# Kernel optimization log

Hardware: AMD Instinct MI355X
Metric: run time of the kernel (lower is better)

## Reference

```python
import jax, jax.numpy as jnp
import numpy as np

EPS = 1e-12

def l2norm(x, axis):
    # torch.nn.functional.normalize: x / max(||x||_2, eps)
    n = jnp.sqrt(jnp.sum(x * x, axis=axis, keepdims=True))
    return x / jnp.maximum(n, EPS)

def setup_inputs() -> dict:
    key = jax.random.key(0)
    k1, k2, k3, k4 = jax.random.split(key, 4)
    B, Cf, H, W = 128, 1024, 16, 16
    n_att, dv = 312, 300
    img = jax.random.normal(k1, (B, Cf, H, W), dtype=jnp.float32)
    # V is initialized from row-normalized w2v embeddings in the module
    V = l2norm(jax.random.normal(k2, (n_att, dv), dtype=jnp.float32), axis=1)
    W1 = jax.random.normal(k3, (dv, Cf), dtype=jnp.float32)
    W2 = jax.random.normal(k4, (dv, Cf), dtype=jnp.float32)
    return {"img": img, "V": V, "W1": W1, "W2": W2}

def reference(img, V, W1, W2):
    vv = l2norm(V, axis=1)                               # [i, v]
    B, Cf, H, Wd = img.shape
    av = l2norm(img.reshape(B, Cf, H * Wd), axis=1)      # [b, f, r]
    Q = vv @ W1                                          # [i, f]
    A = jnp.einsum('if,bfr->bir', Q, av)                 # attention logits
    A = jax.nn.softmax(A, axis=-1)
    F_p = jnp.einsum('bir,bfr->bif', A, av)              # attended features
    Pred_att = jnp.einsum('if,bif->bi', vv @ W2, F_p)
    return Pred_att
```

## Files before the change

### kernel.cpp

```cpp
#include <hip/hip_runtime.h>
#include <math.h>

#define NB   128
#define CF   1024
#define RR   256
#define NA   312
#define DV   300
#define MT   640
#define NKC  32
#define NQ   160

typedef _Float16 half8  __attribute__((ext_vector_type(8)));
typedef _Float16 half4  __attribute__((ext_vector_type(4)));
typedef float float16v  __attribute__((ext_vector_type(16)));
typedef float float4v   __attribute__((ext_vector_type(4)));

__device__ __forceinline__ void gll16(const void* g, void* l) {
    __builtin_amdgcn_global_load_lds(
        (const __attribute__((address_space(1))) void*)g,
        (__attribute__((address_space(3))) void*)l, 16, 0, 0);
}

__launch_bounds__(256, 4)
__global__ void k_prep(const float* __restrict__ img, float* __restrict__ ssq32,
                       _Float16* __restrict__ avT) {
    int m  = blockIdx.x;
    int kc = m & 31;
    int b  = m >> 5;
    int t  = threadIdx.x;
    __shared__ __align__(16) float tile[32][256];

    const char* src = (const char*)(img + ((size_t)b * CF + kc * 32) * RR);
    #pragma unroll
    for (int i = 0; i < 8; ++i)
        gll16(src + (size_t)i * 4096 + (size_t)t * 16,
              (char*)tile + i * 4096 + t * 16);
    asm volatile("s_waitcnt vmcnt(0)" ::: "memory");
    __syncthreads();

    float v[32];
    #pragma unroll
    for (int f = 0; f < 32; ++f) v[f] = tile[f][t];
    float ss = 0.f;
    #pragma unroll
    for (int f = 0; f < 32; ++f) ss += v[f] * v[f];

    _Float16* dst = avT + ((size_t)(b * NKC + kc) * RR + t) * 32;
    #pragma unroll
    for (int s = 0; s < 4; ++s) {
        half8 o;
        #pragma unroll
        for (int j = 0; j < 8; ++j) o[j] = (_Float16)v[s * 8 + j];
        *(half8*)(dst + s * 8) = o;
    }
    ssq32[(size_t)(b * NKC + kc) * RR + t] = ss;
}

__launch_bounds__(256, 4)
__global__ void k_q(const float* __restrict__ V, const float* __restrict__ W1,
                    const float* __restrict__ W2, _Float16* __restrict__ Qb) {
    int ib = blockIdx.x;
    int t  = threadIdx.x;
    bool isQ2 = ib >= 80;
    int i0l = (ib - (isQ2 ? 80 : 0)) * 4;
    __shared__ float inv4[4];
    float acc[4][4];
    #pragma unroll
    for (int ii = 0; ii < 4; ++ii)
        #pragma unroll
        for (int j = 0; j < 4; ++j) acc[ii][j] = 0.f;
    if (i0l < NA) {
        int row = t >> 6, l64 = t & 63;
        float s = 0.f;
        for (int v = l64; v < DV; v += 64) { float x = V[(i0l + row) * DV + v]; s += x * x; }
        #pragma unroll
        for (int o = 32; o; o >>= 1) s += __shfl_xor(s, o, 64);
        if (l64 == 0) inv4[row] = 1.f / fmaxf(sqrtf(s), 1e-12f);
        __syncthreads();
        const float* W  = isQ2 ? W2 : W1;
        const float* Vb = V + (size_t)i0l * DV;
        for (int v = 0; v < DV; v += 2) {
            float4v w0 = *(const float4v*)(W + (size_t)v * CF + t * 4);
            float4v w1 = *(const float4v*)(W + (size_t)(v + 1) * CF + t * 4);
            #pragma unroll
            for (int ii = 0; ii < 4; ++ii) {
                float a0 = Vb[(size_t)ii * DV + v];
                float a1 = Vb[(size_t)ii * DV + v + 1];
                #pragma unroll
                for (int j = 0; j < 4; ++j) acc[ii][j] += a0 * w0[j] + a1 * w1[j];
            }
        }
        #pragma unroll
        for (int ii = 0; ii < 4; ++ii)
            #pragma unroll
            for (int j = 0; j < 4; ++j) acc[ii][j] *= inv4[ii];
    }
    int fg = t >> 3;
    int fo = (t & 7) * 4;
    int q12 = isQ2 ? 1 : 0;
    #pragma unroll
    for (int ii = 0; ii < 4; ++ii) {
        half4 h;
        #pragma unroll
        for (int j = 0; j < 4; ++j) h[j] = (_Float16)acc[ii][j];
        *(half4*)&Qb[((size_t)fg * MT + (2 * (i0l + ii) + q12)) * 32 + fo] = h;
    }
}

extern __shared__ char smem[];
__launch_bounds__(512, 2)
__global__ void k_gemm(const _Float16* __restrict__ Qb, const _Float16* __restrict__ avT,
                       const float* __restrict__ ssq32, float* __restrict__ out) {
    int lin = blockIdx.x;
    int xcd = lin & 7;
    int u   = lin >> 3;
    int b   = xcd + 8 * (u & 15);
    int t2h = u >> 4;

    int tid  = threadIdx.x;
    int lane = tid & 63;
    int w    = tid >> 6;
    int wm   = w >> 2;
    int wn   = w & 3;
    int nl   = lane & 31;
    int kh   = lane >> 5;

    int c1 = 512 + tid;
    int a_s0 = (tid % 320) * 64 + (tid / 320) * 16;
    int a_s1 = (c1 % 320) * 64 + (c1 / 320) * 16;
    int a_s2 = ((tid & 255) + 64) * 64 + 3 * 16;
    int a_d0 = tid * 16;
    int a_d1 = a_d0 + 8192;
    int a_d2 = 16384 + (tid & 255) * 16;
    int b_s0 = (tid & 255) * 64 + (tid >> 8) * 16;

    const char* Abase_g = (const char*)Qb;
    const char* Bbase_g = (const char*)avT + ((size_t)b * NKC) * RR * 64;

    float16v acc[5][2];
    #pragma unroll
    for (int i = 0; i < 5; ++i)
        #pragma unroll
        for (int j = 0; j < 2; ++j)
            #pragma unroll
            for (int gi = 0; gi < 16; ++gi) acc[i][j][gi] = 0.f;

    char* p0 = smem;
    char* p1 = smem + 36864;
    char* p2 = smem + 73728;

    #define STAGE(kc_, buf) do {                                                   \
        int kcl = (kc_) < NKC ? (kc_) : (NKC - 1);                                 \
        const char* aS = Abase_g + ((size_t)kcl * MT + (size_t)t2h * 320) * 64;    \
        const char* bS = Bbase_g + (size_t)kcl * RR * 64;                          \
        char* ab = (buf); char* bb = (buf) + 20480;                                \
        gll16(aS + a_s0, ab + a_d0);                                               \
        gll16(aS + a_s1, ab + a_d1);                                               \
        gll16(aS + a_s2, ab + a_d2);                                               \
        gll16(bS + b_s0,      bb + tid * 16);                                      \
        gll16(bS + b_s0 + 32, bb + tid * 16 + 8192);                               \
    } while (0)

    #define COMPUTE(buf) do {                                                      \
        const char* Al = (buf); const char* Bl = (buf) + 20480;                    \
        _Pragma("unroll")                                                          \
        for (int ks = 0; ks < 2; ++ks) {                                           \
            int kb = ks * 2 + kh;                                                  \
            half8 bf0 = *(const half8*)(Bl + ((size_t)kb * 256 + wn * 64 + nl) * 16);      \
            half8 bf1 = *(const half8*)(Bl + ((size_t)kb * 256 + wn * 64 + 32 + nl) * 16); \
            _Pragma("unroll")                                                      \
            for (int mt = 0; mt < 5; ++mt) {                                       \
                half8 af = *(const half8*)(Al + ((size_t)kb * 320 + wm * 160 + mt * 32 + nl) * 16); \
                acc[mt][0] = __builtin_amdgcn_mfma_f32_32x32x16_f16(af, bf0, acc[mt][0], 0, 0, 0);  \
                acc[mt][1] = __builtin_amdgcn_mfma_f32_32x32x16_f16(af, bf1, acc[mt][1], 0, 0, 0);  \
            }                                                                      \
        }                                                                          \
    } while (0)

    STAGE(0, p0);
    __builtin_amdgcn_sched_barrier(0);
    STAGE(1, p1);
    asm volatile("s_waitcnt vmcnt(5)" ::: "memory");
    __builtin_amdgcn_s_barrier();
    __builtin_amdgcn_sched_barrier(0);

    #pragma unroll 1
    for (int kc = 0; kc < NKC; ++kc) {
        STAGE(kc + 2, p2);
        asm volatile("s_waitcnt vmcnt(5)" ::: "memory");
        __builtin_amdgcn_sched_barrier(0);
        COMPUTE(p0);
        __builtin_amdgcn_sched_barrier(0);
        __builtin_amdgcn_s_barrier();
        char* tmp = p0; p0 = p1; p1 = p2; p2 = tmp;
    }
    asm volatile("s_waitcnt vmcnt(0)" ::: "memory");
    __builtin_amdgcn_s_barrier();
    __builtin_amdgcn_sched_barrier(0);
    #undef STAGE
    #undef COMPUTE

    float* mred = (float*)smem;
    float* mg   = (float*)(smem + 2560);
    float* sred = (float*)(smem + 3200);
    float* dred = (float*)(smem + 5760);

    const float* sq = ssq32 + (size_t)b * NKC * RR;
    int c0 = wn * 64 + nl;
    float q0 = 0.f, q1 = 0.f;
    #pragma unroll
    for (int kc = 0; kc < NKC; ++kc) {
        q0 += sq[(size_t)kc * RR + c0];
        q1 += sq[(size_t)kc * RR + 32 + c0];
    }
    float iv0 = 1.f / fmaxf(sqrtf(q0), 1e-12f);
    float iv1 = 1.f / fmaxf(sqrtf(q1), 1e-12f);
    #pragma unroll
    for (int mt = 0; mt < 5; ++mt)
        #pragma unroll
        for (int gi = 0; gi < 16; ++gi) {
            acc[mt][0][gi] *= iv0;
            acc[mt][1][gi] *= iv1;
        }

    #pragma unroll
    for (int mt = 0; mt < 5; ++mt) {
        #pragma unroll
        for (int e = 0; e < 8; ++e) {
            int g = 2 * e;
            float mx = fmaxf(acc[mt][0][g], acc[mt][1][g]);
            #pragma unroll
            for (int off = 1; off <= 16; off <<= 1)
                mx = fmaxf(mx, __shfl_xor(mx, off, 64));
            if (nl == 0) {
                int row = (g & 3) + 8 * (g >> 2) + 4 * kh;
                mred[wn * 160 + wm * 80 + mt * 16 + (row >> 1)] = mx;
            }
        }
    }
    __syncthreads();
    if (tid < 160)
        mg[tid] = fmaxf(fmaxf(mred[tid], mred[160 + tid]),
                        fmaxf(mred[320 + tid], mred[480 + tid]));
    __syncthreads();

    #pragma unroll
    for (int mt = 0; mt < 5; ++mt) {
        #pragma unroll
        for (int e = 0; e < 8; ++e) {
            int g = 2 * e;
            int row = (g & 3) + 8 * (g >> 2) + 4 * kh;
            int Pl = wm * 80 + mt * 16 + (row >> 1);
            float m = mg[Pl];
            float e0 = __expf(acc[mt][0][g] - m);
            float e1 = __expf(acc[mt][1][g] - m);
            float s = e0 + e1;
            float d = e0 * acc[mt][0][g + 1] + e1 * acc[mt][1][g + 1];
            #pragma unroll
            for (int off = 1; off <= 16; off <<= 1) {
                s += __shfl_xor(s, off, 64);
                d += __shfl_xor(d, off, 64);
            }
            if (nl == 0) {
                sred[wn * 160 + Pl] = s;
                dred[wn * 160 + Pl] = d;
            }
        }
    }
    __syncthreads();
    if (tid < 160) {
        float s = sred[tid] + sred[160 + tid] + sred[320 + tid] + sred[480 + tid];
        float d = dred[tid] + dred[160 + tid] + dred[320 + tid] + dred[480 + tid];
        int ig = t2h * 160 + tid;
        if (ig < NA) out[b * NA + ig] = d / s;
    }
}

extern "C" void kernel_launch(void* const* d_in, const int* in_sizes, int n_in,
                              void* d_out, int out_size, void* d_ws, size_t ws_size,
                              hipStream_t stream) {
    const float* img = (const float*)d_in[0];
    const float* V   = (const float*)d_in[1];
    const float* W1  = (const float*)d_in[2];
    const float* W2  = (const float*)d_in[3];
    float* out = (float*)d_out;

    char* ws = (char*)d_ws;
    size_t off = 0;
    float*    ssq32 = (float*)(ws + off);    off += (size_t)NB * NKC * RR * 4;
    _Float16* avT   = (_Float16*)(ws + off); off += (size_t)NB * CF * RR * 2;
    _Float16* Qb    = (_Float16*)(ws + off); off += (size_t)NKC * MT * 32 * 2;

    static bool attr_done = false;
    if (!attr_done) {
        hipFuncSetAttribute((const void*)k_gemm,
                            hipFuncAttributeMaxDynamicSharedMemorySize, 110592);
        attr_done = true;
    }

    k_prep<<<dim3(NB * NKC), 256, 0, stream>>>(img, ssq32, avT);
    k_q<<<dim3(NQ), 256, 0, stream>>>(V, W1, W2, Qb);
    k_gemm<<<dim3(256), 512, 110592, stream>>>(Qb, avT, ssq32, out);
}
```

Before: 298.5 us.

## Fuse img fp16 conversion and norm into GEMM with split-R softmax combine

Removes the prep kernel that wrote an fp16 transposed copy of img plus per-chunk sums of squares. The GEMM kernel now streams fp32 img directly into LDS, converts it to fp16 in registers, and accumulates the column sums of squares itself. Each block now covers all 640 Q rows but only half of the 256 spatial positions. A small combine kernel merges the two halves' partial softmax max, sum and dot values. This saves a full write and re-read of the fp16 intermediate but doubles LDS traffic for B, adds scalar LDS reads and conversions to the inner loop, and drops from triple to double buffering.

```diff
diff --git a/kernel.cpp b/kernel.cpp
--- a/kernel.cpp
+++ b/kernel.cpp
@@ -9,6 +9,10 @@
 #define MT   640
 #define NKC  32
 #define NQ   160
+#define NPI  320
+#define ABYTES 40960
+#define BBYTES 16384
+#define BUFSZ  57344
 
 typedef _Float16 half8  __attribute__((ext_vector_type(8)));
 typedef _Float16 half4  __attribute__((ext_vector_type(4)));
@@ -19,41 +23,6 @@
     __builtin_amdgcn_global_load_lds(
         (const __attribute__((address_space(1))) void*)g,
         (__attribute__((address_space(3))) void*)l, 16, 0, 0);
-}
-
-__launch_bounds__(256, 4)
-__global__ void k_prep(const float* __restrict__ img, float* __restrict__ ssq32,
-                       _Float16* __restrict__ avT) {
-    int m  = blockIdx.x;
-    int kc = m & 31;
-    int b  = m >> 5;
-    int t  = threadIdx.x;
-    __shared__ __align__(16) float tile[32][256];
-
-    const char* src = (const char*)(img + ((size_t)b * CF + kc * 32) * RR);
-    #pragma unroll
-    for (int i = 0; i < 8; ++i)
-        gll16(src + (size_t)i * 4096 + (size_t)t * 16,
-              (char*)tile + i * 4096 + t * 16);
-    asm volatile("s_waitcnt vmcnt(0)" ::: "memory");
-    __syncthreads();
-
-    float v[32];
-    #pragma unroll
-    for (int f = 0; f < 32; ++f) v[f] = tile[f][t];
-    float ss = 0.f;
-    #pragma unroll
-    for (int f = 0; f < 32; ++f) ss += v[f] * v[f];
-
-    _Float16* dst = avT + ((size_t)(b * NKC + kc) * RR + t) * 32;
-    #pragma unroll
-    for (int s = 0; s < 4; ++s) {
-        half8 o;
-        #pragma unroll
-        for (int j = 0; j < 8; ++j) o[j] = (_Float16)v[s * 8 + j];
-        *(half8*)(dst + s * 8) = o;
-    }
-    ssq32[(size_t)(b * NKC + kc) * RR + t] = ss;
 }
 
 __launch_bounds__(256, 4)
@@ -109,33 +78,35 @@
 
 extern __shared__ char smem[];
 __launch_bounds__(512, 2)
-__global__ void k_gemm(const _Float16* __restrict__ Qb, const _Float16* __restrict__ avT,
-                       const float* __restrict__ ssq32, float* __restrict__ out) {
+__global__ void k_fused(const float* __restrict__ img, const _Float16* __restrict__ Qb,
+                        float* __restrict__ pm, float* __restrict__ ps,
+                        float* __restrict__ pd) {
     int lin = blockIdx.x;
-    int xcd = lin & 7;
-    int u   = lin >> 3;
-    int b   = xcd + 8 * (u & 15);
-    int t2h = u >> 4;
+    int b   = lin >> 1;
+    int rh  = lin & 1;
 
     int tid  = threadIdx.x;
     int lane = tid & 63;
     int w    = tid >> 6;
-    int wm   = w >> 2;
-    int wn   = w & 3;
+    int wm   = w >> 1;
+    int wn   = w & 1;
     int nl   = lane & 31;
     int kh   = lane >> 5;
 
-    int c1 = 512 + tid;
-    int a_s0 = (tid % 320) * 64 + (tid / 320) * 16;
-    int a_s1 = (c1 % 320) * 64 + (c1 / 320) * 16;
-    int a_s2 = ((tid & 255) + 64) * 64 + 3 * 16;
-    int a_d0 = tid * 16;
-    int a_d1 = a_d0 + 8192;
-    int a_d2 = 16384 + (tid & 255) * 16;
-    int b_s0 = (tid & 255) * 64 + (tid >> 8) * 16;
-
-    const char* Abase_g = (const char*)Qb;
-    const char* Bbase_g = (const char*)avT + ((size_t)b * NKC) * RR * 64;
+    int aG[5];
+    #pragma unroll
+    for (int j = 0; j < 5; ++j) {
+        int s = tid + j * 512;
+        aG[j] = ((s % 640) * 4 + (s / 640)) * 16;
+    }
+    int bG[2];
+    #pragma unroll
+    for (int j = 0; j < 2; ++j) {
+        int s = tid + j * 512;
+        bG[j] = (s >> 5) * (RR * 4) + (s & 31) * 16;
+    }
+    const char* gA = (const char*)Qb;
+    const char* gB = (const char*)img + ((size_t)b * CF * RR + (size_t)rh * 128) * 4;
 
     float16v acc[5][2];
     #pragma unroll
@@ -144,55 +115,67 @@
         for (int j = 0; j < 2; ++j)
             #pragma unroll
             for (int gi = 0; gi < 16; ++gi) acc[i][j][gi] = 0.f;
-
-    char* p0 = smem;
-    char* p1 = smem + 36864;
-    char* p2 = smem + 73728;
-
-    #define STAGE(kc_, buf) do {                                                   \
+    float ssq = 0.f;
+
+    #define STAGE(kc_) do {                                                        \
         int kcl = (kc_) < NKC ? (kc_) : (NKC - 1);                                 \
-        const char* aS = Abase_g + ((size_t)kcl * MT + (size_t)t2h * 320) * 64;    \
-        const char* bS = Bbase_g + (size_t)kcl * RR * 64;                          \
-        char* ab = (buf); char* bb = (buf) + 20480;                                \
-        gll16(aS + a_s0, ab + a_d0);                                               \
-        gll16(aS + a_s1, ab + a_d1);                                               \
-        gll16(aS + a_s2, ab + a_d2);                                               \
-        gll16(bS + b_s0,      bb + tid * 16);                                      \
-        gll16(bS + b_s0 + 32, bb + tid * 16 + 8192);                               \
+        char* buf = smem + (((kc_) & 1) ? BUFSZ : 0);                              \
+        const char* aS = gA + (size_t)kcl * ABYTES;                                \
+        const char* bS = gB + (size_t)kcl * 32768;                                 \
+        _Pragma("unroll")                                                          \
+        for (int j = 0; j < 5; ++j) gll16(aS + aG[j], buf + (tid + j * 512) * 16); \
+        _Pragma("unroll")                                                          \
+        for (int j = 0; j < 2; ++j)                                                \
+            gll16(bS + bG[j], buf + ABYTES + (tid + j * 512) * 16);                \
     } while (0)
 
-    #define COMPUTE(buf) do {                                                      \
-        const char* Al = (buf); const char* Bl = (buf) + 20480;                    \
+    #define COMPUTE(kc_) do {                                                      \
+        char* buf = smem + (((kc_) & 1) ? BUFSZ : 0);                              \
+        const char* Al = buf; const char* Bl = buf + ABYTES;                       \
+        int c0 = wn * 64 + nl;                                                     \
         _Pragma("unroll")                                                          \
         for (int ks = 0; ks < 2; ++ks) {                                           \
             int kb = ks * 2 + kh;                                                  \
-            half8 bf0 = *(const half8*)(Bl + ((size_t)kb * 256 + wn * 64 + nl) * 16);      \
-            half8 bf1 = *(const half8*)(Bl + ((size_t)kb * 256 + wn * 64 + 32 + nl) * 16); \
+            float bv0[8], bv1[8];                                                  \
+            _Pragma("unroll")                                                      \
+            for (int j = 0; j < 8; ++j) {                                          \
+                bv0[j] = *(const float*)(Bl + (((kb * 8 + j) * 128) + c0) * 4);    \
+                bv1[j] = *(const float*)(Bl + (((kb * 8 + j) * 128) + c0 + 32) * 4); \
+            }                                                                      \
+            half8 bf0, bf1;                                                        \
+            _Pragma("unroll")                                                      \
+            for (int j = 0; j < 8; ++j) {                                          \
+                bf0[j] = (_Float16)bv0[j]; bf1[j] = (_Float16)bv1[j];              \
+            }                                                                      \
             _Pragma("unroll")                                                      \
             for (int mt = 0; mt < 5; ++mt) {                                       \
-                half8 af = *(const half8*)(Al + ((size_t)kb * 320 + wm * 160 + mt * 32 + nl) * 16); \
+                half8 af = *(const half8*)(Al + ((size_t)kb * 640 + wm * 160 + mt * 32 + nl) * 16); \
                 acc[mt][0] = __builtin_amdgcn_mfma_f32_32x32x16_f16(af, bf0, acc[mt][0], 0, 0, 0);  \
                 acc[mt][1] = __builtin_amdgcn_mfma_f32_32x32x16_f16(af, bf1, acc[mt][1], 0, 0, 0);  \
             }                                                                      \
         }                                                                          \
     } while (0)
 
-    STAGE(0, p0);
-    __builtin_amdgcn_sched_barrier(0);
-    STAGE(1, p1);
-    asm volatile("s_waitcnt vmcnt(5)" ::: "memory");
-    __builtin_amdgcn_s_barrier();
-    __builtin_amdgcn_sched_barrier(0);
-
+    STAGE(0);
     #pragma unroll 1
     for (int kc = 0; kc < NKC; ++kc) {
-        STAGE(kc + 2, p2);
-        asm volatile("s_waitcnt vmcnt(5)" ::: "memory");
+        STAGE(kc + 1);
+        asm volatile("s_waitcnt vmcnt(7)" ::: "memory");
+        __builtin_amdgcn_s_barrier();
         __builtin_amdgcn_sched_barrier(0);
-        COMPUTE(p0);
+        COMPUTE(kc);
+        {
+            if (tid < 128) {
+                const char* Bl = smem + ((kc & 1) ? BUFSZ : 0) + ABYTES;
+                #pragma unroll
+                for (int f = 0; f < 32; ++f) {
+                    float x = *(const float*)(Bl + (f * 128 + tid) * 4);
+                    ssq += x * x;
+                }
+            }
+        }
         __builtin_amdgcn_sched_barrier(0);
         __builtin_amdgcn_s_barrier();
-        char* tmp = p0; p0 = p1; p1 = p2; p2 = tmp;
     }
     asm volatile("s_waitcnt vmcnt(0)" ::: "memory");
     __builtin_amdgcn_s_barrier();
@@ -200,21 +183,17 @@
     #undef STAGE
     #undef COMPUTE
 
-    float* mred = (float*)smem;
-    float* mg   = (float*)(smem + 2560);
-    float* sred = (float*)(smem + 3200);
-    float* dred = (float*)(smem + 5760);
-
-    const float* sq = ssq32 + (size_t)b * NKC * RR;
+    float* ssq_lds = (float*)smem;
+    float* mred    = (float*)(smem + 512);
+    float* mg      = (float*)(smem + 3072);
+    float* sred    = (float*)(smem + 4352);
+    float* dred    = (float*)(smem + 6912);
+
+    if (tid < 128) ssq_lds[tid] = ssq;
+    __syncthreads();
     int c0 = wn * 64 + nl;
-    float q0 = 0.f, q1 = 0.f;
-    #pragma unroll
-    for (int kc = 0; kc < NKC; ++kc) {
-        q0 += sq[(size_t)kc * RR + c0];
-        q1 += sq[(size_t)kc * RR + 32 + c0];
-    }
-    float iv0 = 1.f / fmaxf(sqrtf(q0), 1e-12f);
-    float iv1 = 1.f / fmaxf(sqrtf(q1), 1e-12f);
+    float iv0 = 1.f / fmaxf(sqrtf(ssq_lds[c0]), 1e-12f);
+    float iv1 = 1.f / fmaxf(sqrtf(ssq_lds[c0 + 32]), 1e-12f);
     #pragma unroll
     for (int mt = 0; mt < 5; ++mt)
         #pragma unroll
@@ -234,14 +213,12 @@
                 mx = fmaxf(mx, __shfl_xor(mx, off, 64));
             if (nl == 0) {
                 int row = (g & 3) + 8 * (g >> 2) + 4 * kh;
-                mred[wn * 160 + wm * 80 + mt * 16 + (row >> 1)] = mx;
-            }
-        }
-    }
-    __syncthreads();
-    if (tid < 160)
-        mg[tid] = fmaxf(fmaxf(mred[tid], mred[160 + tid]),
-                        fmaxf(mred[320 + tid], mred[480 + tid]));
+                mred[wn * NPI + wm * 80 + mt * 16 + (row >> 1)] = mx;
+            }
+        }
+    }
+    __syncthreads();
+    if (tid < NPI) mg[tid] = fmaxf(mred[tid], mred[NPI + tid]);
     __syncthreads();
 
     #pragma unroll
@@ -250,8 +227,8 @@
         for (int e = 0; e < 8; ++e) {
             int g = 2 * e;
             int row = (g & 3) + 8 * (g >> 2) + 4 * kh;
-            int Pl = wm * 80 + mt * 16 + (row >> 1);
-            float m = mg[Pl];
+            int i   = wm * 80 + mt * 16 + (row >> 1);
+            float m  = mg[i];
             float e0 = __expf(acc[mt][0][g] - m);
             float e1 = __expf(acc[mt][1][g] - m);
             float s = e0 + e1;
@@ -262,18 +239,33 @@
                 d += __shfl_xor(d, off, 64);
             }
             if (nl == 0) {
-                sred[wn * 160 + Pl] = s;
-                dred[wn * 160 + Pl] = d;
-            }
-        }
-    }
-    __syncthreads();
-    if (tid < 160) {
-        float s = sred[tid] + sred[160 + tid] + sred[320 + tid] + sred[480 + tid];
-        float d = dred[tid] + dred[160 + tid] + dred[320 + tid] + dred[480 + tid];
-        int ig = t2h * 160 + tid;
-        if (ig < NA) out[b * NA + ig] = d / s;
-    }
+                sred[wn * NPI + i] = s;
+                dred[wn * NPI + i] = d;
+            }
+        }
+    }
+    __syncthreads();
+    if (tid < NPI) {
+        size_t pb = ((size_t)b * 2 + rh) * NPI + tid;
+        pm[pb] = mg[tid];
+        ps[pb] = sred[tid] + sred[NPI + tid];
+        pd[pb] = dred[tid] + dred[NPI + tid];
+    }
+}
+
+__launch_bounds__(256, 4)
+__global__ void k_comb(const float* __restrict__ pm, const float* __restrict__ ps,
+                       const float* __restrict__ pd, float* __restrict__ out) {
+    int idx = blockIdx.x * 256 + threadIdx.x;
+    int b = idx / NPI;
+    int i = idx - b * NPI;
+    float m0 = pm[(size_t)(b * 2) * NPI + i];
+    float m1 = pm[(size_t)(b * 2 + 1) * NPI + i];
+    float m  = fmaxf(m0, m1);
+    float w0 = __expf(m0 - m), w1 = __expf(m1 - m);
+    float s = ps[(size_t)(b * 2) * NPI + i] * w0 + ps[(size_t)(b * 2 + 1) * NPI + i] * w1;
+    float d = pd[(size_t)(b * 2) * NPI + i] * w0 + pd[(size_t)(b * 2 + 1) * NPI + i] * w1;
+    if (i < NA) out[(size_t)b * NA + i] = d / s;
 }
 
 extern "C" void kernel_launch(void* const* d_in, const int* in_sizes, int n_in,
@@ -287,18 +279,19 @@
 
     char* ws = (char*)d_ws;
     size_t off = 0;
-    float*    ssq32 = (float*)(ws + off);    off += (size_t)NB * NKC * RR * 4;
-    _Float16* avT   = (_Float16*)(ws + off); off += (size_t)NB * CF * RR * 2;
-    _Float16* Qb    = (_Float16*)(ws + off); off += (size_t)NKC * MT * 32 * 2;
+    _Float16* Qb = (_Float16*)(ws + off); off += (size_t)NKC * MT * 32 * 2;
+    float*    pm = (float*)(ws + off);    off += (size_t)NB * 2 * NPI * 4;
+    float*    ps = (float*)(ws + off);    off += (size_t)NB * 2 * NPI * 4;
+    float*    pd = (float*)(ws + off);    off += (size_t)NB * 2 * NPI * 4;
 
     static bool attr_done = false;
     if (!attr_done) {
-        hipFuncSetAttribute((const void*)k_gemm,
-                            hipFuncAttributeMaxDynamicSharedMemorySize, 110592);
+        hipFuncSetAttribute((const void*)k_fused,
+                            hipFuncAttributeMaxDynamicSharedMemorySize, 2 * BUFSZ);
         attr_done = true;
     }
 
-    k_prep<<<dim3(NB * NKC), 256, 0, stream>>>(img, ssq32, avT);
     k_q<<<dim3(NQ), 256, 0, stream>>>(V, W1, W2, Qb);
-    k_gemm<<<dim3(256), 512, 110592, stream>>>(Qb, avT, ssq32, out);
-}
+    k_fused<<<dim3(256), 512, 2 * BUFSZ, stream>>>(img, Qb, pm, ps, pd);
+    k_comb<<<dim3(160), 256, 0, stream>>>(pm, ps, pd, out);
+}
```

Result: faster. 264.3 us (-11.4%).
